# Optimization experiments

Hardware: AMD Instinct MI355X
Metric: run time of the kernel (lower is better)

The kernel has to match this reference:

```python
import jax, jax.numpy as jnp
import numpy as np

GROUP_SIZE = 128
OUT_F, IN_F = 4096, 4096
B, S = 4, 2048


@jax.custom_vjp
def ste_sign(x):
    return jnp.sign(x)

def _ste_fwd(x):
    return jnp.sign(x), None

def _ste_bwd(_, g):
    return (g,)  # straight-through: identity gradient

ste_sign.defvjp(_ste_fwd, _ste_bwd)


def setup_inputs() -> dict:
    key = jax.random.key(0)
    k1, k2, k3 = jax.random.split(key, 3)
    x = jax.random.normal(k1, (B, S, IN_F), dtype=jnp.float32)
    # sign weights are +/-1.0 (zeros mapped to +1, as in the torch init)
    sw = jnp.sign(jax.random.normal(k2, (OUT_F, IN_F), dtype=jnp.float32))
    sign_weights = jnp.where(sw == 0, 1.0, sw)
    # frozen per-group scales (mean |w| per group of 128); positive values
    scales = jax.random.uniform(k3, (OUT_F * IN_F // GROUP_SIZE,), dtype=jnp.float32,
                                minval=0.005, maxval=0.05)
    return {"x": x, "sign_weights": sign_weights, "scales": scales}


def reference(x, sign_weights, scales):
    # binary = sign(sign_weights) with STE (identity grad)
    binary = ste_sign(sign_weights)
    # expand per-group scales: repeat each scale GROUP_SIZE times, view as (out, in)
    scale_mat = jnp.repeat(scales, GROUP_SIZE).reshape(OUT_F, IN_F)
    weight = binary * scale_mat  # [out_f, in_f]
    # F.linear(x, weight) = x @ weight.T
    return jnp.einsum('bsi,oi->bso', x, weight.astype(x.dtype))
```

## Files before the change

### kernel.cpp

```cpp
#include <hip/hip_runtime.h>

#define K_DIM 4096
#define N_DIM 4096
#define M_DIM 8192

typedef __bf16 bf16;
typedef __attribute__((ext_vector_type(8))) __bf16 bf16x8;
typedef __attribute__((ext_vector_type(16))) float f32x16;
typedef __attribute__((ext_vector_type(8))) unsigned short u16x8;

__device__ inline unsigned short f2bf(float f) {
    unsigned u = __builtin_bit_cast(unsigned, f);
    u += 0x7fffu + ((u >> 16) & 1u);
    return (unsigned short)(u >> 16);
}

__global__ __launch_bounds__(256) void prep_kernel(const float* __restrict__ x,
                                                   const float* __restrict__ sw,
                                                   const float* __restrict__ scales,
                                                   unsigned short* __restrict__ oA,
                                                   unsigned short* __restrict__ oW) {
    const int b = blockIdx.x;
    if (b < 16384) {
        const size_t i = (size_t)b * 256 + threadIdx.x;
        const float4* p = (const float4*)x + i * 2;
        float4 a = p[0], c = p[1];
        u16x8 v;
        v[0] = f2bf(a.x); v[1] = f2bf(a.y); v[2] = f2bf(a.z); v[3] = f2bf(a.w);
        v[4] = f2bf(c.x); v[5] = f2bf(c.y); v[6] = f2bf(c.z); v[7] = f2bf(c.w);
        *((u16x8*)oA + i) = v;
    } else {
        const size_t i = (size_t)(b - 16384) * 256 + threadIdx.x;
        const float s = scales[i >> 4];
        const float4* p = (const float4*)sw + i * 2;
        float4 a = p[0], c = p[1];
        u16x8 v;
        v[0] = f2bf(a.x * s); v[1] = f2bf(a.y * s); v[2] = f2bf(a.z * s); v[3] = f2bf(a.w * s);
        v[4] = f2bf(c.x * s); v[5] = f2bf(c.y * s); v[6] = f2bf(c.z * s); v[7] = f2bf(c.w * s);
        *((u16x8*)oW + i) = v;
    }
}

__device__ inline void gll16(const bf16* g, bf16* l) {
    __builtin_amdgcn_global_load_lds(
        (const __attribute__((address_space(1))) void*)g,
        (__attribute__((address_space(3))) void*)l, 16, 0, 0);
}

__global__ __launch_bounds__(256, 2) void gemm_bt_kernel(const bf16* __restrict__ A,
                                                         const bf16* __restrict__ W,
                                                         float* __restrict__ C) {
    __shared__ bf16 As[256 * 64];
    __shared__ bf16 Bs[128 * 64];

    const int t = threadIdx.x;
    const int m0 = blockIdx.y * 256;
    const int n0 = blockIdx.x * 128;
    const int lane = t & 63;
    const int w = t >> 6;
    const int wm = (w >> 1) * 128;
    const int wn = (w & 1) * 64;
    const int ln = lane & 31;
    const int hl = lane >> 5;

    f32x16 acc[4][2] = {};

    const int srow = t >> 3;
    const int scol = (t & 7) ^ (srow & 7);
    const bf16* ga = A + (size_t)(m0 + srow) * K_DIM + scol * 8;
    const bf16* gb = W + (size_t)(n0 + srow) * K_DIM + scol * 8;
    bf16* la = As + t * 8;
    bf16* lb = Bs + t * 8;

    int co[4];
#pragma unroll
    for (int ks = 0; ks < 4; ++ks) co[ks] = ((ks * 2 + hl) ^ (ln & 7)) * 8;
    const bf16* paRow = As + (wm + ln) * 64;
    const bf16* pbRow = Bs + (wn + ln) * 64;

    for (int kb = 0; kb < K_DIM; kb += 64) {
#pragma unroll
        for (int j = 0; j < 8; ++j)
            gll16(ga + kb + (size_t)(32 * j) * K_DIM, la + j * 2048);
#pragma unroll
        for (int j = 0; j < 4; ++j)
            gll16(gb + kb + (size_t)(32 * j) * K_DIM, lb + j * 2048);
        __syncthreads();

#pragma unroll
        for (int ks = 0; ks < 4; ++ks) {
            bf16x8 af[4], bfr[2];
#pragma unroll
            for (int mi = 0; mi < 4; ++mi)
                af[mi] = *(const bf16x8*)(paRow + mi * 2048 + co[ks]);
#pragma unroll
            for (int ni = 0; ni < 2; ++ni)
                bfr[ni] = *(const bf16x8*)(pbRow + ni * 2048 + co[ks]);
#pragma unroll
            for (int mi = 0; mi < 4; ++mi)
#pragma unroll
                for (int ni = 0; ni < 2; ++ni)
                    acc[mi][ni] = __builtin_amdgcn_mfma_f32_32x32x16_bf16(
                        af[mi], bfr[ni], acc[mi][ni], 0, 0, 0);
        }
        __syncthreads();
    }

    float* Cb = C + (size_t)(m0 + wm) * N_DIM + n0 + wn;
#pragma unroll
    for (int mi = 0; mi < 4; ++mi)
#pragma unroll
        for (int ni = 0; ni < 2; ++ni)
#pragma unroll
            for (int r = 0; r < 16; ++r) {
                const int row = mi * 32 + (r & 3) + 8 * (r >> 2) + 4 * hl;
                Cb[(size_t)row * N_DIM + ni * 32 + ln] = acc[mi][ni][r];
            }
}

extern "C" void kernel_launch(void* const* d_in, const int* in_sizes, int n_in,
                              void* d_out, int out_size, void* d_ws, size_t ws_size,
                              hipStream_t stream) {
    const float* x      = (const float*)d_in[0];
    const float* sw     = (const float*)d_in[1];
    const float* scales = (const float*)d_in[2];
    float* out = (float*)d_out;

    bf16* Abf = (bf16*)d_ws;
    bf16* Wbf = (bf16*)((char*)d_ws + (size_t)M_DIM * K_DIM * 2);

    prep_kernel<<<24576, 256, 0, stream>>>(x, sw, scales,
                                           (unsigned short*)Abf, (unsigned short*)Wbf);

    dim3 grid(N_DIM / 128, M_DIM / 256);
    gemm_bt_kernel<<<grid, 256, 0, stream>>>(Abf, Wbf, out);
}
```

Baseline: 517.0 us.

## Rewrite GEMM as 256x256 double-buffered pipelined kernel with 16x16 MFMA

Replaces the single-buffered 256x128 tile GEMM with a 512-thread, 256x256 tile kernel that double-buffers K slices in 128KB of dynamic LDS. Global-to-LDS loads are interleaved with MFMA phases and controlled by explicit vmcnt/lgkmcnt waits, barriers and setprio. It also switches to 16x16x32 MFMA, adds a block-index swizzle for L2 locality, and makes the prep kernel grid-stride with fewer blocks. The goal is to hide memory latency and raise MFMA utilization, at the cost of complex hand-tuned synchronization and higher LDS use that may limit occupancy.

Result: faster. 492.3 us (-4.8%).

```diff
diff --git a/kernel.cpp b/kernel.cpp
--- a/kernel.cpp
+++ b/kernel.cpp
@@ -3,10 +3,11 @@
 #define K_DIM 4096
 #define N_DIM 4096
 #define M_DIM 8192
+#define NT 64
 
 typedef __bf16 bf16;
 typedef __attribute__((ext_vector_type(8))) __bf16 bf16x8;
-typedef __attribute__((ext_vector_type(16))) float f32x16;
+typedef __attribute__((ext_vector_type(4))) float f32x4;
 typedef __attribute__((ext_vector_type(8))) unsigned short u16x8;
 
 __device__ inline unsigned short f2bf(float f) {
@@ -20,20 +21,23 @@
                                                    const float* __restrict__ scales,
                                                    unsigned short* __restrict__ oA,
                                                    unsigned short* __restrict__ oW) {
-    const int b = blockIdx.x;
-    if (b < 16384) {
-        const size_t i = (size_t)b * 256 + threadIdx.x;
+    const unsigned T = blockIdx.x * 256u + threadIdx.x;
+#pragma unroll
+    for (int k = 0; k < 8; ++k) {
+        const size_t i = (size_t)k * 524288u + T;
         const float4* p = (const float4*)x + i * 2;
-        float4 a = p[0], c = p[1];
+        const float4 a = p[0], c = p[1];
         u16x8 v;
         v[0] = f2bf(a.x); v[1] = f2bf(a.y); v[2] = f2bf(a.z); v[3] = f2bf(a.w);
         v[4] = f2bf(c.x); v[5] = f2bf(c.y); v[6] = f2bf(c.z); v[7] = f2bf(c.w);
         *((u16x8*)oA + i) = v;
-    } else {
-        const size_t i = (size_t)(b - 16384) * 256 + threadIdx.x;
+    }
+#pragma unroll
+    for (int k = 0; k < 4; ++k) {
+        const size_t i = (size_t)k * 524288u + T;
         const float s = scales[i >> 4];
         const float4* p = (const float4*)sw + i * 2;
-        float4 a = p[0], c = p[1];
+        const float4 a = p[0], c = p[1];
         u16x8 v;
         v[0] = f2bf(a.x * s); v[1] = f2bf(a.y * s); v[2] = f2bf(a.z * s); v[3] = f2bf(a.w * s);
         v[4] = f2bf(c.x * s); v[5] = f2bf(c.y * s); v[6] = f2bf(c.z * s); v[7] = f2bf(c.w * s);
@@ -47,91 +51,151 @@
         (__attribute__((address_space(3))) void*)l, 16, 0, 0);
 }
 
-__global__ __launch_bounds__(256, 2) void gemm_bt_kernel(const bf16* __restrict__ A,
+extern __shared__ bf16 lds[];
+
+__global__ __launch_bounds__(512, 2) void gemm_bt_kernel(const bf16* __restrict__ A,
                                                          const bf16* __restrict__ W,
                                                          float* __restrict__ C) {
-    __shared__ bf16 As[256 * 64];
-    __shared__ bf16 Bs[128 * 64];
+    const int raw = blockIdx.x;
+    const int swz = (raw & 7) * 64 + (raw >> 3);
+    const int m0 = (swz >> 4) * 256;
+    const int n0 = (swz & 15) * 256;
 
     const int t = threadIdx.x;
-    const int m0 = blockIdx.y * 256;
-    const int n0 = blockIdx.x * 128;
     const int lane = t & 63;
     const int w = t >> 6;
-    const int wm = (w >> 1) * 128;
-    const int wn = (w & 1) * 64;
-    const int ln = lane & 31;
-    const int hl = lane >> 5;
-
-    f32x16 acc[4][2] = {};
-
-    const int srow = t >> 3;
-    const int scol = (t & 7) ^ (srow & 7);
-    const bf16* ga = A + (size_t)(m0 + srow) * K_DIM + scol * 8;
-    const bf16* gb = W + (size_t)(n0 + srow) * K_DIM + scol * 8;
-    bf16* la = As + t * 8;
-    bf16* lb = Bs + t * 8;
-
-    int co[4];
-#pragma unroll
-    for (int ks = 0; ks < 4; ++ks) co[ks] = ((ks * 2 + hl) ^ (ln & 7)) * 8;
-    const bf16* paRow = As + (wm + ln) * 64;
-    const bf16* pbRow = Bs + (wn + ln) * 64;
-
-    for (int kb = 0; kb < K_DIM; kb += 64) {
-#pragma unroll
-        for (int j = 0; j < 8; ++j)
-            gll16(ga + kb + (size_t)(32 * j) * K_DIM, la + j * 2048);
-#pragma unroll
-        for (int j = 0; j < 4; ++j)
-            gll16(gb + kb + (size_t)(32 * j) * K_DIM, lb + j * 2048);
-        __syncthreads();
-
-#pragma unroll
-        for (int ks = 0; ks < 4; ++ks) {
-            bf16x8 af[4], bfr[2];
-#pragma unroll
-            for (int mi = 0; mi < 4; ++mi)
-                af[mi] = *(const bf16x8*)(paRow + mi * 2048 + co[ks]);
-#pragma unroll
-            for (int ni = 0; ni < 2; ++ni)
-                bfr[ni] = *(const bf16x8*)(pbRow + ni * 2048 + co[ks]);
-#pragma unroll
-            for (int mi = 0; mi < 4; ++mi)
-#pragma unroll
-                for (int ni = 0; ni < 2; ++ni)
-                    acc[mi][ni] = __builtin_amdgcn_mfma_f32_32x32x16_bf16(
-                        af[mi], bfr[ni], acc[mi][ni], 0, 0, 0);
-        }
-        __syncthreads();
-    }
-
-    float* Cb = C + (size_t)(m0 + wm) * N_DIM + n0 + wn;
-#pragma unroll
-    for (int mi = 0; mi < 4; ++mi)
-#pragma unroll
-        for (int ni = 0; ni < 2; ++ni)
-#pragma unroll
-            for (int r = 0; r < 16; ++r) {
-                const int row = mi * 32 + (r & 3) + 8 * (r >> 2) + 4 * hl;
-                Cb[(size_t)row * N_DIM + ni * 32 + ln] = acc[mi][ni][r];
-            }
+    const int wm = w >> 2;
+    const int wn = w & 3;
+
+    const int srow = t >> 2;
+    const int slb = ((t & 3) ^ ((t >> 3) & 3)) * 8;
+    const bf16* gA = A + (size_t)(m0 + srow) * K_DIM + slb;
+    const bf16* gB = W + (size_t)(n0 + srow) * K_DIM + slb;
+    bf16* lA = lds + t * 8;
+    bf16* lB = lds + 16384 + t * 8;
+
+    const int r = lane & 15;
+    const int be8 = ((lane >> 4) ^ ((lane >> 1) & 3)) * 8;
+    const bf16* fA = lds + (wm * 128 + r) * 32 + be8;
+    const bf16* fB = lds + 16384 + (wn * 64 + r) * 32 + be8;
+
+    f32x4 acc[8][4] = {};
+    bf16x8 af[8], b0, b1;
+
+#define STAGE(gbase, kofs, ldst)                                       \
+    do {                                                               \
+        gll16((gbase) + (kofs), (ldst));                               \
+        gll16((gbase) + (size_t)128 * K_DIM + (kofs), (ldst) + 4096);  \
+    } while (0)
+
+#define BAR __builtin_amdgcn_s_barrier()
+#define LGKM0                                                   \
+    do {                                                        \
+        asm volatile("s_waitcnt lgkmcnt(0)" ::: "memory");      \
+        __builtin_amdgcn_sched_barrier(0);                      \
+    } while (0)
+
+#define MFMA_HALF(NIB)                                                               \
+    do {                                                                             \
+        _Pragma("unroll") for (int mi = 0; mi < 8; ++mi) {                           \
+            acc[mi][NIB] = __builtin_amdgcn_mfma_f32_16x16x32_bf16(                  \
+                af[mi], b0, acc[mi][NIB], 0, 0, 0);                                  \
+            acc[mi][(NIB) + 1] = __builtin_amdgcn_mfma_f32_16x16x32_bf16(            \
+                af[mi], b1, acc[mi][(NIB) + 1], 0, 0, 0);                            \
+        }                                                                            \
+    } while (0)
+
+#define GROUP(BUF, I1, I2, VMC6, VMC0)                                               \
+    do {                                                                             \
+                                                           \
+        _Pragma("unroll") for (int mi = 0; mi < 8; ++mi)                             \
+            af[mi] = *(const bf16x8*)(fA + (BUF)*32768 + mi * 512);                  \
+        b0 = *(const bf16x8*)(fB + (BUF)*32768 + 0 * 512);                           \
+        b1 = *(const bf16x8*)(fB + (BUF)*32768 + 1 * 512);                           \
+        if (I1) STAGE(gB, ko1, lB + (1 - (BUF)) * 32768 + 8192);                     \
+        BAR; LGKM0;                                                                  \
+        __builtin_amdgcn_s_setprio(1); MFMA_HALF(0); __builtin_amdgcn_s_setprio(0);  \
+        BAR;                                                                         \
+                                                           \
+        b0 = *(const bf16x8*)(fB + (BUF)*32768 + 2 * 512);                           \
+        b1 = *(const bf16x8*)(fB + (BUF)*32768 + 3 * 512);                           \
+        if (I2) STAGE(gA, ko2, lA + (BUF)*32768);                                    \
+        BAR; LGKM0;                                                                  \
+        __builtin_amdgcn_s_setprio(1); MFMA_HALF(2); __builtin_amdgcn_s_setprio(0);  \
+        BAR;                                                                         \
+                                                           \
+        _Pragma("unroll") for (int mi = 0; mi < 8; ++mi)                             \
+            af[mi] = *(const bf16x8*)(fA + (BUF)*32768 + 8192 + mi * 512);           \
+        b0 = *(const bf16x8*)(fB + (BUF)*32768 + 8192 + 0 * 512);                    \
+        b1 = *(const bf16x8*)(fB + (BUF)*32768 + 8192 + 1 * 512);                    \
+        if (I2) STAGE(gB, ko2, lB + (BUF)*32768);                                    \
+        BAR; LGKM0;                                                                  \
+        __builtin_amdgcn_s_setprio(1); MFMA_HALF(0); __builtin_amdgcn_s_setprio(0);  \
+        BAR;                                                                         \
+                                                           \
+        b0 = *(const bf16x8*)(fB + (BUF)*32768 + 8192 + 2 * 512);                    \
+        b1 = *(const bf16x8*)(fB + (BUF)*32768 + 8192 + 3 * 512);                    \
+        if (I2) STAGE(gA, ko2 + 32, lA + (BUF)*32768 + 8192);                        \
+        BAR; LGKM0;                                                                  \
+        __builtin_amdgcn_s_setprio(1); MFMA_HALF(2); __builtin_amdgcn_s_setprio(0);  \
+        if (VMC6) asm volatile("s_waitcnt vmcnt(6)" ::: "memory");                   \
+        if (VMC0) asm volatile("s_waitcnt vmcnt(0)" ::: "memory");                   \
+        BAR;                                                                         \
+    } while (0)
+
+    STAGE(gA, 0, lA);
+    STAGE(gB, 0, lB);
+    STAGE(gA, 32, lA + 8192);
+    STAGE(gB, 32, lB + 8192);
+    STAGE(gA, 64, lA + 32768);
+    STAGE(gB, 64, lB + 32768);
+    STAGE(gA, 96, lA + 32768 + 8192);
+    asm volatile("s_waitcnt vmcnt(6)" ::: "memory");
+    BAR;
+
+    int ko1 = 96;
+    int ko2 = 128;
+#pragma unroll 1
+    for (int gg = 0; gg < 31; ++gg) {
+        GROUP(0, true, true, true, false);
+        ko1 += 64; ko2 += 64;
+        GROUP(1, true, true, true, false);
+        ko1 += 64; ko2 += 64;
+    }
+    GROUP(0, true, false, false, true);
+    GROUP(1, false, false, false, false);
+
+    const int cr = lane >> 4;
+    float* Cb = C + (size_t)(m0 + wm * 128 + cr * 4) * N_DIM + (n0 + wn * 64 + r);
+#pragma unroll
+    for (int mi = 0; mi < 8; ++mi)
+#pragma unroll
+        for (int ni = 0; ni < 4; ++ni)
+#pragma unroll
+            for (int q = 0; q < 4; ++q)
+                Cb[(size_t)(mi * 16 + q) * N_DIM + ni * 16] = acc[mi][ni][q];
 }
 
 extern "C" void kernel_launch(void* const* d_in, const int* in_sizes, int n_in,
                               void* d_out, int out_size, void* d_ws, size_t ws_size,
                               hipStream_t stream) {
-    const float* x      = (const float*)d_in[0];
-    const float* sw     = (const float*)d_in[1];
+    const float* x = (const float*)d_in[0];
+    const float* sw = (const float*)d_in[1];
     const float* scales = (const float*)d_in[2];
     float* out = (float*)d_out;
 
     bf16* Abf = (bf16*)d_ws;
     bf16* Wbf = (bf16*)((char*)d_ws + (size_t)M_DIM * K_DIM * 2);
 
-    prep_kernel<<<24576, 256, 0, stream>>>(x, sw, scales,
-                                           (unsigned short*)Abf, (unsigned short*)Wbf);
-
-    dim3 grid(N_DIM / 128, M_DIM / 256);
-    gemm_bt_kernel<<<grid, 256, 0, stream>>>(Abf, Wbf, out);
-}
+    static int lds_set = 0;
+    if (!lds_set) {
+        hipFuncSetAttribute((const void*)gemm_bt_kernel,
+                            hipFuncAttributeMaxDynamicSharedMemorySize, 131072);
+        lds_set = 1;
+    }
+
+    prep_kernel<<<2048, 256, 0, stream>>>(x, sw, scales,
+                                          (unsigned short*)Abf, (unsigned short*)Wbf);
+
+    gemm_bt_kernel<<<dim3(N_DIM / 256 * (M_DIM / 256)), 512, 131072, stream>>>(Abf, Wbf, out);
+}
```
